# Performance work log

Hardware: AMD Instinct MI355X
Metric: run time of the kernel (lower is better)

The kernel has to match this reference:

```python
import jax, jax.numpy as jnp
import numpy as np

B, H, S, F_RANK, DV = 8, 8, 2048, 64, 64
NEG = -1e9


def setup_inputs() -> dict:
    key = jax.random.key(0)
    k1, k2, k3, k4 = jax.random.split(key, 4)
    v = jax.random.normal(k1, (B, H, S, DV), dtype=jnp.float32)
    mask = jax.random.randint(k2, (B, 1, S, S), 0, 2, dtype=jnp.int32)
    random_attn_1 = jax.random.normal(k3, (B, H, S, F_RANK), dtype=jnp.float32)
    random_attn_2 = jax.random.normal(k4, (B, H, F_RANK, S), dtype=jnp.float32)
    return {
        "v": v,
        "mask": mask,
        "random_attn_1": random_attn_1,
        "random_attn_2": random_attn_2,
        "len_q": S,
    }


def reference(v, mask, random_attn_1, random_attn_2, len_q):
    # low-rank factor matmul -> [B, H, S, S] scores
    nb = mask.shape[0]
    a1 = random_attn_1[:nb, :, :len_q, :]   # [B, H, Lq, f]
    a2 = random_attn_2[:nb, :, :, :len_q]   # [B, H, f, Lq]
    scores = jnp.einsum('bhsf,bhft->bhst', a1, a2)
    scores = jnp.where(mask == 0, NEG, scores)
    attn = jax.nn.softmax(scores, axis=-1)  # dropout rate 0.0 -> identity
    out = jnp.einsum('bhst,bhtd->bhsd', attn, v)
    return out, attn
```

## Files before the change

### kernel.cpp

```cpp
#include <hip/hip_runtime.h>
#include <hip/hip_bf16.h>

#define S_DIM 2048
#define DV_DIM 64
#define NEGV (-1000000000.0f)

typedef __bf16 bf16x8 __attribute__((ext_vector_type(8)));
typedef float  f32x4  __attribute__((ext_vector_type(4)));

#define MFMA(a, b, c) __builtin_amdgcn_mfma_f32_16x16x32_bf16(a, b, c, 0, 0, 0)

__global__ __launch_bounds__(512, 2)
void fra_kernel(const float* __restrict__ vptr,
                const int*   __restrict__ mask,
                const float* __restrict__ a1,
                const float* __restrict__ a2,
                float* __restrict__ out,
                float* __restrict__ attn)
{
    const int tid  = threadIdx.x;
    const int wv   = tid >> 6;
    const int lane = tid & 63;
    const int q    = lane >> 4;
    const int ln   = lane & 15;

    const int idx  = blockIdx.x;
    const int w    = (idx & 7) * 1024 + (idx >> 3);
    const int bh   = w >> 7;
    const int row0 = (w & 127) << 4;

    __shared__ float redmax[8][16];
    __shared__ float redsum[8][16];
    __shared__ __align__(16) __bf16 pbuf[8][16][136];

    const float* a1p = a1 + ((size_t)bh * S_DIM + row0 + ln) * 64 + q * 8;
    bf16x8 a1hi[2], a1lo[2];
#pragma unroll
    for (int kb = 0; kb < 2; ++kb) {
        const float4 f0 = *(const float4*)(a1p + kb * 32);
        const float4 f1 = *(const float4*)(a1p + kb * 32 + 4);
        float tf[8] = {f0.x, f0.y, f0.z, f0.w, f1.x, f1.y, f1.z, f1.w};
#pragma unroll
        for (int j = 0; j < 8; ++j) {
            __bf16 h = (__bf16)tf[j];
            __bf16 l = (__bf16)(tf[j] - (float)h);
            a1hi[kb][j] = h;
            a1lo[kb][j] = l;
        }
    }

    f32x4 acc[16];
#pragma unroll
    for (int ct = 0; ct < 16; ++ct) acc[ct] = f32x4{0.f, 0.f, 0.f, 0.f};

    const int cbase = wv * 256;
    const float* a2p = a2 + (size_t)bh * 64 * S_DIM + (size_t)(q * 8) * S_DIM + ln;

#pragma unroll
    for (int ct = 0; ct < 16; ++ct) {
        const int c0 = cbase + ct * 16;
        bf16x8 bhi[2], blo[2];
#pragma unroll
        for (int kb = 0; kb < 2; ++kb) {
#pragma unroll
            for (int j = 0; j < 8; ++j) {
                float fv = a2p[(size_t)(kb * 32 + j) * S_DIM + c0];
                __bf16 h = (__bf16)fv;
                __bf16 l = (__bf16)(fv - (float)h);
                bhi[kb][j] = h;
                blo[kb][j] = l;
            }
        }
        acc[ct] = MFMA(a1hi[0], bhi[0], acc[ct]);
        acc[ct] = MFMA(a1hi[1], bhi[1], acc[ct]);
        acc[ct] = MFMA(a1lo[0], bhi[0], acc[ct]);
        acc[ct] = MFMA(a1lo[1], bhi[1], acc[ct]);
        acc[ct] = MFMA(a1hi[0], blo[0], acc[ct]);
        acc[ct] = MFMA(a1hi[1], blo[1], acc[ct]);
    }

    const int* mp = mask + ((size_t)(bh >> 3) * S_DIM + row0 + q * 4) * S_DIM + cbase + ln;
    float lmax[4] = {NEGV, NEGV, NEGV, NEGV};
#pragma unroll
    for (int ct = 0; ct < 16; ++ct) {
#pragma unroll
        for (int rr = 0; rr < 4; ++rr) {
            int mv = mp[(size_t)rr * S_DIM + ct * 16];
            float s = mv ? acc[ct][rr] : NEGV;
            acc[ct][rr] = s;
            lmax[rr] = fmaxf(lmax[rr], s);
        }
    }
#pragma unroll
    for (int off = 8; off >= 1; off >>= 1) {
#pragma unroll
        for (int rr = 0; rr < 4; ++rr)
            lmax[rr] = fmaxf(lmax[rr], __shfl_xor(lmax[rr], off, 64));
    }
    if (ln == 0) {
#pragma unroll
        for (int rr = 0; rr < 4; ++rr) redmax[wv][q * 4 + rr] = lmax[rr];
    }
    __syncthreads();
    float rmax[4];
#pragma unroll
    for (int rr = 0; rr < 4; ++rr) {
        float m = redmax[0][q * 4 + rr];
#pragma unroll
        for (int w8 = 1; w8 < 8; ++w8) m = fmaxf(m, redmax[w8][q * 4 + rr]);
        rmax[rr] = m;
    }

    float lsum[4] = {0.f, 0.f, 0.f, 0.f};
#pragma unroll
    for (int ct = 0; ct < 16; ++ct) {
#pragma unroll
        for (int rr = 0; rr < 4; ++rr) {
            float p = __expf(acc[ct][rr] - rmax[rr]);
            acc[ct][rr] = p;
            lsum[rr] += p;
        }
    }
#pragma unroll
    for (int off = 8; off >= 1; off >>= 1) {
#pragma unroll
        for (int rr = 0; rr < 4; ++rr)
            lsum[rr] += __shfl_xor(lsum[rr], off, 64);
    }
    if (ln == 0) {
#pragma unroll
        for (int rr = 0; rr < 4; ++rr) redsum[wv][q * 4 + rr] = lsum[rr];
    }
    __syncthreads();
    float rinv[4];
#pragma unroll
    for (int rr = 0; rr < 4; ++rr) {
        float s2 = redsum[0][q * 4 + rr];
#pragma unroll
        for (int w8 = 1; w8 < 8; ++w8) s2 += redsum[w8][q * 4 + rr];
        rinv[rr] = 1.0f / s2;
    }

    float* attnp = attn + ((size_t)bh * S_DIM + row0 + q * 4) * S_DIM + cbase + ln;
    const float* vp = vptr + (size_t)bh * S_DIM * DV_DIM + (size_t)(cbase + q * 8) * DV_DIM + ln;

    f32x4 oacc[4];
#pragma unroll
    for (int nt = 0; nt < 4; ++nt) oacc[nt] = f32x4{0.f, 0.f, 0.f, 0.f};

#pragma unroll
    for (int ch = 0; ch < 2; ++ch) {
#pragma unroll
        for (int t8 = 0; t8 < 8; ++t8) {
            const int ct = ch * 8 + t8;
#pragma unroll
            for (int rr = 0; rr < 4; ++rr) {
                float a = acc[ct][rr] * rinv[rr];
                attnp[(size_t)rr * S_DIM + ct * 16] = a;
                pbuf[wv][q * 4 + rr][t8 * 16 + ln] = (__bf16)a;
            }
        }
        __syncthreads();
#pragma unroll
        for (int kc = 0; kc < 4; ++kc) {
            bf16x8 af = *(const bf16x8*)&pbuf[wv][ln][kc * 32 + q * 8];
#pragma unroll
            for (int nt = 0; nt < 4; ++nt) {
                bf16x8 bf;
#pragma unroll
                for (int j = 0; j < 8; ++j)
                    bf[j] = (__bf16)vp[(size_t)(ch * 128 + kc * 32 + j) * DV_DIM + nt * 16];
                oacc[nt] = MFMA(af, bf, oacc[nt]);
            }
        }
        __syncthreads();
    }

    float* ob = (float*)&pbuf[wv][0][0];
#pragma unroll
    for (int nt = 0; nt < 4; ++nt) {
#pragma unroll
        for (int rr = 0; rr < 4; ++rr)
            ob[(q * 4 + rr) * 68 + nt * 16 + ln] = oacc[nt][rr];
    }
    __syncthreads();

#pragma unroll
    for (int i = 0; i < 2; ++i) {
        int e = tid + i * 512;
        int r = e >> 6, c = e & 63;
        float s = 0.f;
#pragma unroll
        for (int w8 = 0; w8 < 8; ++w8)
            s += ((const float*)&pbuf[w8][0][0])[r * 68 + c];
        out[((size_t)bh * S_DIM + row0 + r) * DV_DIM + c] = s;
    }
}

extern "C" void kernel_launch(void* const* d_in, const int* in_sizes, int n_in,
                              void* d_out, int out_size, void* d_ws, size_t ws_size,
                              hipStream_t stream) {
    const float* v    = (const float*)d_in[0];
    const int*   mask = (const int*)d_in[1];
    const float* a1   = (const float*)d_in[2];
    const float* a2   = (const float*)d_in[3];

    float* out  = (float*)d_out;
    float* attn = out + (size_t)8 * 8 * 2048 * 64;

    fra_kernel<<<8192, 512, 0, stream>>>(v, mask, a1, a2, out, attn);
}
```

Baseline: 1.923 ms.

## Prepack a2, V and mask into bf16/bitmask layouts before main attention kernel

Adds pre-pass kernels that split a2 into transposed bf16 hi/lo planes, transpose V to bf16, and compress the int32 mask into bitmasks in workspace. The main kernel then does vector loads of MFMA operands and reads 1 bit per mask entry instead of 4 bytes. It also computes the transposed score tile so attn rows can be written with 16-byte nontemporal stores, and it drops the syncthreads around the per-wave pbuf. This costs extra launches and workspace traffic, and falls back to the old kernel if the workspace is too small.

```diff
diff --git a/kernel.cpp b/kernel.cpp
--- a/kernel.cpp
+++ b/kernel.cpp
@@ -6,17 +6,259 @@
 #define NEGV (-1000000000.0f)
 
 typedef __bf16 bf16x8 __attribute__((ext_vector_type(8)));
+typedef __bf16 bf16x4 __attribute__((ext_vector_type(4)));
 typedef float  f32x4  __attribute__((ext_vector_type(4)));
+typedef unsigned short u16;
+typedef u16 u16x8 __attribute__((ext_vector_type(8)));
 
 #define MFMA(a, b, c) __builtin_amdgcn_mfma_f32_16x16x32_bf16(a, b, c, 0, 0, 0)
 
+__global__ __launch_bounds__(256)
+void pack_a2_kernel(const float* __restrict__ a2,
+                    u16* __restrict__ hi, u16* __restrict__ lo)
+{
+    const int bh = blockIdx.x >> 5;
+    const int tb = (blockIdx.x & 31) << 6;
+    __shared__ u16 sh[64][65];
+    __shared__ u16 sl[64][65];
+    const float* src = a2 + (size_t)bh * 64 * S_DIM + tb;
+    const int tid = threadIdx.x;
+#pragma unroll
+    for (int i = 0; i < 16; ++i) {
+        int e = tid + i * 256;
+        int f = e >> 6, c = e & 63;
+        float v = src[(size_t)f * S_DIM + c];
+        __bf16 h = (__bf16)v;
+        __bf16 l = (__bf16)(v - (float)h);
+        union { __bf16 b; u16 u; } ch_, cl_;
+        ch_.b = h; cl_.b = l;
+        sh[c][f] = ch_.u;
+        sl[c][f] = cl_.u;
+    }
+    __syncthreads();
+    const int r = tid >> 2, k0 = (tid & 3) << 4;
+    u16x8 h0, h1, l0, l1;
+#pragma unroll
+    for (int j = 0; j < 8; ++j) {
+        h0[j] = sh[r][k0 + j]; h1[j] = sh[r][k0 + 8 + j];
+        l0[j] = sl[r][k0 + j]; l1[j] = sl[r][k0 + 8 + j];
+    }
+    size_t off = ((size_t)bh * S_DIM + tb + r) * 64 + k0;
+    *(u16x8*)(hi + off) = h0; *(u16x8*)(hi + off + 8) = h1;
+    *(u16x8*)(lo + off) = l0; *(u16x8*)(lo + off + 8) = l1;
+}
+
+__global__ __launch_bounds__(256)
+void pack_v_kernel(const float* __restrict__ v, u16* __restrict__ vT)
+{
+    const int bh = blockIdx.x >> 5;
+    const int tb = (blockIdx.x & 31) << 6;
+    __shared__ u16 sv[64][65];
+    const int tid = threadIdx.x;
+#pragma unroll
+    for (int i = 0; i < 16; ++i) {
+        int e = tid + i * 256;
+        int t = e >> 6, d = e & 63;
+        float x = v[((size_t)bh * S_DIM + tb + t) * 64 + d];
+        union { __bf16 b; u16 u; } cv_;
+        cv_.b = (__bf16)x;
+        sv[d][t] = cv_.u;
+    }
+    __syncthreads();
+    const int r = tid >> 2, c0 = (tid & 3) << 4;
+    u16x8 t0v, t1v;
+#pragma unroll
+    for (int j = 0; j < 8; ++j) { t0v[j] = sv[r][c0 + j]; t1v[j] = sv[r][c0 + 8 + j]; }
+    size_t off = ((size_t)bh * 64 + r) * S_DIM + tb + c0;
+    *(u16x8*)(vT + off) = t0v; *(u16x8*)(vT + off + 8) = t1v;
+}
+
+__global__ __launch_bounds__(256)
+void pack_mask_kernel(const int* __restrict__ mask, unsigned int* __restrict__ mbits)
+{
+    const int row = blockIdx.x;
+    const int tid = threadIdx.x;
+    const int wv = tid >> 6, lane = tid & 63;
+    const int* mp = mask + (size_t)row * S_DIM;
+#pragma unroll
+    for (int it = 0; it < 8; ++it) {
+        int c = it * 256 + wv * 64 + lane;
+        unsigned long long b = __ballot(mp[c] != 0);
+        if (lane == 0) {
+            mbits[(size_t)row * 64 + it * 8 + wv * 2]     = (unsigned int)b;
+            mbits[(size_t)row * 64 + it * 8 + wv * 2 + 1] = (unsigned int)(b >> 32);
+        }
+    }
+}
+
 __global__ __launch_bounds__(512, 2)
-void fra_kernel(const float* __restrict__ vptr,
-                const int*   __restrict__ mask,
-                const float* __restrict__ a1,
-                const float* __restrict__ a2,
-                float* __restrict__ out,
-                float* __restrict__ attn)
+void fra_main(const u16* __restrict__ a2hi, const u16* __restrict__ a2lo,
+              const u16* __restrict__ vT, const unsigned int* __restrict__ mbits,
+              const float* __restrict__ a1,
+              float* __restrict__ out, float* __restrict__ attn)
+{
+    const int tid  = threadIdx.x;
+    const int wv   = tid >> 6;
+    const int lane = tid & 63;
+    const int q    = lane >> 4;
+    const int ln   = lane & 15;
+
+    const int idx  = blockIdx.x;
+    const int w    = (idx & 7) * 1024 + (idx >> 3);
+    const int bh   = w >> 7;
+    const int row0 = (w & 127) << 4;
+
+    __shared__ float redmax[8][16];
+    __shared__ float redsum[8][16];
+    __shared__ __align__(16) __bf16 pbuf[8][16][136];
+
+    const int cbase = wv * 256;
+
+    const float* a1p = a1 + ((size_t)bh * S_DIM + row0 + ln) * 64 + q * 8;
+    bf16x8 a1hi[2], a1lo[2];
+#pragma unroll
+    for (int kb = 0; kb < 2; ++kb) {
+        const float4 f0 = *(const float4*)(a1p + kb * 32);
+        const float4 f1 = *(const float4*)(a1p + kb * 32 + 4);
+        float tf[8] = {f0.x, f0.y, f0.z, f0.w, f1.x, f1.y, f1.z, f1.w};
+#pragma unroll
+        for (int j = 0; j < 8; ++j) {
+            __bf16 h = (__bf16)tf[j];
+            __bf16 l = (__bf16)(tf[j] - (float)h);
+            a1hi[kb][j] = h;
+            a1lo[kb][j] = l;
+        }
+    }
+
+    f32x4 acc[16];
+#pragma unroll
+    for (int ct = 0; ct < 16; ++ct) acc[ct] = f32x4{0.f, 0.f, 0.f, 0.f};
+
+    const u16* ah = a2hi + ((size_t)bh * S_DIM + cbase + ln) * 64 + q * 8;
+    const u16* al = a2lo + ((size_t)bh * S_DIM + cbase + ln) * 64 + q * 8;
+
+#pragma unroll
+    for (int ct = 0; ct < 16; ++ct) {
+        const size_t o = (size_t)ct * 1024;
+        bf16x8 h0 = *(const bf16x8*)(ah + o);
+        bf16x8 h1 = *(const bf16x8*)(ah + o + 32);
+        bf16x8 l0 = *(const bf16x8*)(al + o);
+        bf16x8 l1 = *(const bf16x8*)(al + o + 32);
+        acc[ct] = MFMA(h0, a1hi[0], acc[ct]);
+        acc[ct] = MFMA(h1, a1hi[1], acc[ct]);
+        acc[ct] = MFMA(l0, a1hi[0], acc[ct]);
+        acc[ct] = MFMA(l1, a1hi[1], acc[ct]);
+        acc[ct] = MFMA(h0, a1lo[0], acc[ct]);
+        acc[ct] = MFMA(h1, a1lo[1], acc[ct]);
+    }
+
+    const unsigned int* mbp = mbits + ((size_t)(bh >> 3) * S_DIM + row0 + ln) * 64 + wv * 8;
+    const uint4 mwa = *(const uint4*)mbp;
+    const uint4 mwb = *(const uint4*)(mbp + 4);
+    const unsigned int mw[8] = {mwa.x, mwa.y, mwa.z, mwa.w, mwb.x, mwb.y, mwb.z, mwb.w};
+
+    float lm[4] = {NEGV, NEGV, NEGV, NEGV};
+#pragma unroll
+    for (int ct = 0; ct < 16; ++ct) {
+        const unsigned int nib = mw[ct >> 1] >> (((ct & 1) << 4) + (q << 2));
+#pragma unroll
+        for (int rr = 0; rr < 4; ++rr) {
+            float s = ((nib >> rr) & 1u) ? acc[ct][rr] : NEGV;
+            acc[ct][rr] = s;
+            lm[rr] = fmaxf(lm[rr], s);
+        }
+    }
+    float m0 = fmaxf(fmaxf(lm[0], lm[1]), fmaxf(lm[2], lm[3]));
+    m0 = fmaxf(m0, __shfl_xor(m0, 16, 64));
+    m0 = fmaxf(m0, __shfl_xor(m0, 32, 64));
+    if (lane < 16) redmax[wv][lane] = m0;
+    __syncthreads();
+    float rmax = redmax[0][ln];
+#pragma unroll
+    for (int w8 = 1; w8 < 8; ++w8) rmax = fmaxf(rmax, redmax[w8][ln]);
+
+    float ls[4] = {0.f, 0.f, 0.f, 0.f};
+#pragma unroll
+    for (int ct = 0; ct < 16; ++ct) {
+#pragma unroll
+        for (int rr = 0; rr < 4; ++rr) {
+            float p = __expf(acc[ct][rr] - rmax);
+            acc[ct][rr] = p;
+            ls[rr] += p;
+        }
+    }
+    float s0 = (ls[0] + ls[1]) + (ls[2] + ls[3]);
+    s0 += __shfl_xor(s0, 16, 64);
+    s0 += __shfl_xor(s0, 32, 64);
+    if (lane < 16) redsum[wv][lane] = s0;
+    __syncthreads();
+    float rs = redsum[0][ln];
+#pragma unroll
+    for (int w8 = 1; w8 < 8; ++w8) rs += redsum[w8][ln];
+    const float rinv = 1.0f / rs;
+
+    float* attnp = attn + ((size_t)bh * S_DIM + row0 + ln) * S_DIM + cbase + (q << 2);
+    const u16* vp = vT + ((size_t)bh * 64 + ln) * S_DIM + cbase + q * 8;
+
+    f32x4 oacc[4];
+#pragma unroll
+    for (int nt = 0; nt < 4; ++nt) oacc[nt] = f32x4{0.f, 0.f, 0.f, 0.f};
+
+#pragma unroll
+    for (int ch = 0; ch < 2; ++ch) {
+#pragma unroll
+        for (int t8 = 0; t8 < 8; ++t8) {
+            const int ct = ch * 8 + t8;
+            f32x4 p;
+            bf16x4 pk;
+#pragma unroll
+            for (int rr = 0; rr < 4; ++rr) {
+                float a = acc[ct][rr] * rinv;
+                p[rr]  = a;
+                pk[rr] = (__bf16)a;
+            }
+            __builtin_nontemporal_store(p, (f32x4*)(attnp + ct * 16));
+            *(bf16x4*)&pbuf[wv][ln][t8 * 16 + (q << 2)] = pk;
+        }
+#pragma unroll
+        for (int kc = 0; kc < 4; ++kc) {
+            bf16x8 af = *(const bf16x8*)&pbuf[wv][ln][kc * 32 + q * 8];
+#pragma unroll
+            for (int nt = 0; nt < 4; ++nt) {
+                bf16x8 bfv = *(const bf16x8*)(vp + (size_t)nt * 16 * S_DIM + ch * 128 + kc * 32);
+                oacc[nt] = MFMA(af, bfv, oacc[nt]);
+            }
+        }
+    }
+
+    float* ob = (float*)&pbuf[wv][0][0];
+#pragma unroll
+    for (int nt = 0; nt < 4; ++nt) {
+#pragma unroll
+        for (int rr = 0; rr < 4; ++rr)
+            ob[(q * 4 + rr) * 68 + nt * 16 + ln] = oacc[nt][rr];
+    }
+    __syncthreads();
+
+#pragma unroll
+    for (int i = 0; i < 2; ++i) {
+        int e = tid + i * 512;
+        int r = e >> 6, c = e & 63;
+        float s = 0.f;
+#pragma unroll
+        for (int w8 = 0; w8 < 8; ++w8)
+            s += ((const float*)&pbuf[w8][0][0])[r * 68 + c];
+        out[((size_t)bh * S_DIM + row0 + r) * DV_DIM + c] = s;
+    }
+}
+
+__global__ __launch_bounds__(512, 2)
+void fra_kernel_fb(const float* __restrict__ vptr,
+                   const int*   __restrict__ mask,
+                   const float* __restrict__ a1,
+                   const float* __restrict__ a2,
+                   float* __restrict__ out,
+                   float* __restrict__ attn)
 {
     const int tid  = threadIdx.x;
     const int wv   = tid >> 6;
@@ -208,5 +450,19 @@
     float* out  = (float*)d_out;
     float* attn = out + (size_t)8 * 8 * 2048 * 64;
 
-    fra_kernel<<<8192, 512, 0, stream>>>(v, mask, a1, a2, out, attn);
-}
+    const size_t n_a2 = (size_t)64 * 2048 * 64;
+    const size_t need = n_a2 * 3 * sizeof(u16) + (size_t)8 * 2048 * 64 * sizeof(unsigned int);
+
+    if (ws_size >= need) {
+        u16* a2hi = (u16*)d_ws;
+        u16* a2lo = a2hi + n_a2;
+        u16* vTp  = a2lo + n_a2;
+        unsigned int* mb = (unsigned int*)(vTp + n_a2);
+        pack_a2_kernel<<<2048, 256, 0, stream>>>(a2, a2hi, a2lo);
+        pack_v_kernel<<<2048, 256, 0, stream>>>(v, vTp);
+        pack_mask_kernel<<<16384, 256, 0, stream>>>(mask, mb);
+        fra_main<<<8192, 512, 0, stream>>>(a2hi, a2lo, vTp, mb, a1, out, attn);
+    } else {
+        fra_kernel_fb<<<8192, 512, 0, stream>>>(v, mask, a1, a2, out, attn);
+    }
+}
```

After: 2.053 ms. 6.7% more time.
